# Kernel tuning notes

Measured on AMD Instinct MI355X. Metric: run time of the kernel, lower is better.

Reference implementation:

```python
import jax, jax.numpy as jnp
import numpy as np

EPS = 1e-5

def _layernorm(x, w, b):
    mu = jnp.mean(x, axis=-1, keepdims=True)
    var = jnp.var(x, axis=-1, keepdims=True)
    return (x - mu) * jax.lax.rsqrt(var + EPS) * w + b

def setup_inputs() -> dict:
    key = jax.random.key(0)
    ks = jax.random.split(key, 8)
    N, C = 768, 128
    s = 1.0 / np.sqrt(C)
    return {
        "pair": jax.random.normal(ks[0], (N, N, C), dtype=jnp.float32),
        "ln_in_w": jnp.ones((C,), jnp.float32),
        "ln_in_b": jnp.zeros((C,), jnp.float32),
        "w_proj": jax.random.uniform(ks[1], (2 * C, C), jnp.float32, -s, s),
        "w_gate": jax.random.uniform(ks[2], (2 * C, C), jnp.float32, -s, s),
        "ln_c_w": jnp.ones((C,), jnp.float32),
        "ln_c_b": jnp.zeros((C,), jnp.float32),
        "w_out": jax.random.uniform(ks[3], (C, C), jnp.float32, -s, s),
        "w_glin": jax.random.uniform(ks[4], (C, C), jnp.float32, -s, s),
    }

def reference(pair, ln_in_w, ln_in_b, w_proj, w_gate, ln_c_w, ln_c_b, w_out, w_glin):
    # pair: [N, N, C]
    x = _layernorm(pair, ln_in_w, ln_in_b)          # input LayerNorm
    proj = x @ w_proj.T                              # [N, N, 2C]
    gate = x @ w_gate.T                              # [N, N, 2C]
    pg = proj * jax.nn.sigmoid(gate)                 # gated projection
    # torch reshape([2C,N,N] -> [C,2,N,N]) interleaves channels:
    a = pg[..., 0::2]                                # [N, N, C]
    b = pg[..., 1::2]                                # [N, N, C]
    # outgoing: out[i,j,c] = sum_k a[i,k,c] * b[j,k,c]
    out = jnp.einsum('ikc,jkc->ijc', a, b)           # [N, N, C]
    out = _layernorm(out, ln_c_w, ln_c_b)
    out = out @ w_out.T
    out = out * jax.nn.sigmoid(x @ w_glin.T)         # output gate
    return out
```

## Files before the change

### kernel.cpp

```cpp
#include <hip/hip_runtime.h>
#include <stdint.h>


#define NN_F (768 * 768)

typedef float f32x4 __attribute__((ext_vector_type(4)));
typedef __bf16 bf16x8 __attribute__((ext_vector_type(8)));
typedef unsigned short u16x8 __attribute__((ext_vector_type(8)));

#define AS1 __attribute__((address_space(1)))
#define AS3 __attribute__((address_space(3)))

__device__ __forceinline__ unsigned short f2b(float f) {
  unsigned u = __builtin_bit_cast(unsigned, f);
  u = u + 0x7fffu + ((u >> 16) & 1u);
  return (unsigned short)(u >> 16);
}
__device__ __forceinline__ float b2f(unsigned short s) {
  return __builtin_bit_cast(float, ((unsigned)s) << 16);
}
__device__ __forceinline__ float sigf(float x) {
  return 1.0f / (1.0f + __expf(-x));
}

__global__ __launch_bounds__(256) void k0_weights(
    const float* __restrict__ w_proj, const float* __restrict__ w_gate,
    const float* __restrict__ w_glin, const float* __restrict__ w_out,
    unsigned short* __restrict__ Wcat) {
  int idx = blockIdx.x * 256 + threadIdx.x;
  int r = idx >> 7, k = idx & 127;
  float v;
  if (r < 512) {
    int c = r >> 2, tt = r & 3;
    int row = 2 * c + (tt >> 1);
    v = (tt & 1) ? w_gate[row * 128 + k] : w_proj[row * 128 + k];
  } else if (r < 640) {
    v = w_glin[(r - 512) * 128 + k];
  } else {
    v = w_out[(r - 640) * 128 + k];
  }
  Wcat[idx] = f2b(v);
}

__global__ __launch_bounds__(256) void k1_proj(
    const float* __restrict__ pair, const float* __restrict__ lnw,
    const float* __restrict__ lnb, const unsigned short* __restrict__ Wcat,
    unsigned short* __restrict__ a_t, unsigned short* __restrict__ b_t,
    unsigned short* __restrict__ g) {
  __shared__ float xs[64 * 132];
  __shared__ float red[8][64];
  __shared__ float muA[64], rsA[64];
  __shared__ unsigned short wbuf[32 * 512];

  const int t = threadIdx.x;
  const int l = t & 63, w = t >> 6;
  const int lm = l & 15, lq = l >> 4;
  const size_t p0 = (size_t)blockIdx.x * 64;

  const float* src = pair + p0 * 128;
#pragma unroll
  for (int v = 0; v < 8; ++v) {
    int fi = (v * 256 + t) * 4;
    int p = fi >> 7, c = fi & 127;
    f32x4 d = *(const f32x4*)(src + fi);
    *(f32x4*)&xs[p * 132 + c] = d;
  }
#pragma unroll
  for (int s0 = 0; s0 < 2; ++s0) {
    const int at = w * 2 + s0;
#pragma unroll
    for (int kt = 0; kt < 4; ++kt) {
      const unsigned short* gp =
          Wcat + (size_t)(at * 16 + lm) * 128 + kt * 32 + lq * 8;
      __builtin_amdgcn_global_load_lds((const AS1 void*)gp,
                                       (AS3 void*)(wbuf + (at * 4 + kt) * 512),
                                       16, 0, 0);
    }
  }
  __syncthreads();
  {
    int p = t & 63, q = t >> 6;
    float s1 = 0.f, s2 = 0.f;
#pragma unroll
    for (int cc = 0; cc < 32; ++cc) {
      float x = xs[p * 132 + q * 32 + ((cc + p) & 31)];
      s1 += x;
      s2 += x * x;
    }
    red[q][p] = s1;
    red[q + 4][p] = s2;
  }
  __syncthreads();
  if (t < 64) {
    float s1 = red[0][t] + red[1][t] + red[2][t] + red[3][t];
    float s2 = red[4][t] + red[5][t] + red[6][t] + red[7][t];
    float mu = s1 * (1.f / 128.f);
    float var = s2 * (1.f / 128.f) - mu * mu;
    muA[t] = mu;
    rsA[t] = rsqrtf(var + 1e-5f);
  }
  __syncthreads();
  bf16x8 xfr[4][4];
#pragma unroll
  for (int kt = 0; kt < 4; ++kt) {
    const int ks = kt * 32 + lq * 8;
    f32x4 w0 = *(const f32x4*)&lnw[ks];
    f32x4 w1 = *(const f32x4*)&lnw[ks + 4];
    f32x4 c0 = *(const f32x4*)&lnb[ks];
    f32x4 c1 = *(const f32x4*)&lnb[ks + 4];
#pragma unroll
    for (int pt = 0; pt < 4; ++pt) {
      const int p = pt * 16 + lm;
      float rs = rsA[p], nmu = -muA[p] * rs;
      f32x4 x0 = *(const f32x4*)&xs[p * 132 + ks];
      f32x4 x1 = *(const f32x4*)&xs[p * 132 + ks + 4];
      union { bf16x8 v; __bf16 e[8]; } fr;
#pragma unroll
      for (int j = 0; j < 4; ++j) {
        fr.e[j] = (__bf16)((x0[j] * rs + nmu) * w0[j] + c0[j]);
        fr.e[4 + j] = (__bf16)((x1[j] * rs + nmu) * w1[j] + c1[j]);
      }
      xfr[pt][kt] = fr.v;
    }
  }
  __builtin_amdgcn_sched_barrier(0);
#pragma unroll
  for (int s = 0; s < 10; ++s) {
    if (s >= 2 && s <= 8)
      __builtin_amdgcn_s_waitcnt(0x4f74);
    else if (s == 9)
      __builtin_amdgcn_s_waitcnt(0x0f7c);
    const int at = w * 2 + (s & 1);
    bf16x8 af[4];
#pragma unroll
    for (int kt = 0; kt < 4; ++kt)
      af[kt] = *(const bf16x8*)&wbuf[(at * 4 + kt) * 512 + l * 8];
    __builtin_amdgcn_s_waitcnt(0xc07f);
    __builtin_amdgcn_sched_barrier(0);
    if (s < 8) {
      const int r0n = ((s + 2) >> 1) * 128;
#pragma unroll
      for (int kt = 0; kt < 4; ++kt) {
        const unsigned short* gp =
            Wcat + (size_t)(r0n + at * 16 + lm) * 128 + kt * 32 + lq * 8;
        __builtin_amdgcn_global_load_lds(
            (const AS1 void*)gp, (AS3 void*)(wbuf + (at * 4 + kt) * 512),
            16, 0, 0);
      }
    }
    f32x4 acc[4];
#pragma unroll
    for (int pt = 0; pt < 4; ++pt) acc[pt] = (f32x4){0.f, 0.f, 0.f, 0.f};
#pragma unroll
    for (int pt = 0; pt < 4; ++pt)
#pragma unroll
      for (int kt = 0; kt < 4; ++kt)
        acc[pt] = __builtin_amdgcn_mfma_f32_16x16x32_bf16(af[kt], xfr[pt][kt],
                                                          acc[pt], 0, 0, 0);
    const int wc = s >> 1;
    const int rbase = wc * 128 + at * 16 + lq * 4;
#pragma unroll
    for (int pt = 0; pt < 4; ++pt) {
      f32x4 d = acc[pt];
      size_t point = p0 + pt * 16 + lm;
      if (wc < 4) {
        int c = rbase >> 2;
        a_t[(size_t)c * NN_F + point] = f2b(d[0] * sigf(d[1]));
        b_t[(size_t)c * NN_F + point] = f2b(d[2] * sigf(d[3]));
      } else {
        int co = rbase - 512;
        union { unsigned long long ll; unsigned short u[4]; } pk;
        pk.u[0] = f2b(sigf(d[0]));
        pk.u[1] = f2b(sigf(d[1]));
        pk.u[2] = f2b(sigf(d[2]));
        pk.u[3] = f2b(sigf(d[3]));
        *(unsigned long long*)&g[point * 128 + co] = pk.ll;
      }
    }
  }
}

__global__ __launch_bounds__(256) void k2_einsum(
    const unsigned short* __restrict__ a_t, const unsigned short* __restrict__ b_t,
    unsigned short* __restrict__ o_t) {
  __shared__ unsigned short As[2][128 * 32];
  __shared__ unsigned short Bs[2][128 * 32];
  const int t = threadIdx.x;
  const int l = t & 63, w = t >> 6;
  const int lm = l & 15, lq = l >> 4;
  const int c = blockIdx.z;
  const int m0 = blockIdx.y * 128, n0 = blockIdx.x * 128;
  const unsigned short* Ac = a_t + (size_t)c * NN_F;
  const unsigned short* Bc = b_t + (size_t)c * NN_F;
  const int wi = w >> 1, wj = w & 1;
  const int lrow = l >> 2, lk = (l & 3) * 8;
  f32x4 acc[4][4];
#pragma unroll
  for (int ti = 0; ti < 4; ++ti)
#pragma unroll
    for (int tj = 0; tj < 4; ++tj) acc[ti][tj] = (f32x4){0.f, 0.f, 0.f, 0.f};

  auto stage = [&](int buf, int kb) {
#pragma unroll
    for (int h = 0; h < 2; ++h) {
      int row = w * 32 + h * 16 + lrow;
      __builtin_amdgcn_global_load_lds(
          (const AS1 void*)(Ac + (size_t)(m0 + row) * 768 + kb * 32 + lk),
          (AS3 void*)(As[buf] + (w * 32 + h * 16) * 32), 16, 0, 0);
      __builtin_amdgcn_global_load_lds(
          (const AS1 void*)(Bc + (size_t)(n0 + row) * 768 + kb * 32 + lk),
          (AS3 void*)(Bs[buf] + (w * 32 + h * 16) * 32), 16, 0, 0);
    }
  };

  stage(0, 0);
  int cur = 0;
  for (int kb = 0; kb < 24; ++kb) {
    __syncthreads();
    if (kb < 23) stage(cur ^ 1, kb + 1);
    bf16x8 af[4], bfr[4];
#pragma unroll
    for (int ti = 0; ti < 4; ++ti)
      af[ti] = *(const bf16x8*)&As[cur][(wi * 64 + ti * 16 + lm) * 32 + lq * 8];
#pragma unroll
    for (int tj = 0; tj < 4; ++tj)
      bfr[tj] = *(const bf16x8*)&Bs[cur][(wj * 64 + tj * 16 + lm) * 32 + lq * 8];
#pragma unroll
    for (int ti = 0; ti < 4; ++ti)
#pragma unroll
      for (int tj = 0; tj < 4; ++tj)
        acc[ti][tj] = __builtin_amdgcn_mfma_f32_16x16x32_bf16(
            af[ti], bfr[tj], acc[ti][tj], 0, 0, 0);
    cur ^= 1;
  }
  unsigned short* Oc = o_t + (size_t)c * NN_F;
#pragma unroll
  for (int ti = 0; ti < 4; ++ti) {
    int ib = m0 + wi * 64 + ti * 16 + lq * 4;
#pragma unroll
    for (int tj = 0; tj < 4; ++tj) {
      int j = n0 + wj * 64 + tj * 16 + lm;
      f32x4 d = acc[ti][tj];
#pragma unroll
      for (int r = 0; r < 4; ++r) Oc[(size_t)(ib + r) * 768 + j] = f2b(d[r]);
    }
  }
}

__global__ __launch_bounds__(256) void k3_out(
    const unsigned short* __restrict__ o_t, const float* __restrict__ lnw,
    const float* __restrict__ lnb, const unsigned short* __restrict__ Wcat,
    const unsigned short* __restrict__ g, float* __restrict__ out) {
  __shared__ unsigned short ys[64 * 136];
  __shared__ float red[8][64];
  __shared__ float muA[64], rsA[64];
  __shared__ unsigned short wbuf[32 * 512];

  const int t = threadIdx.x;
  const int l = t & 63, w = t >> 6;
  const int lm = l & 15, lq = l >> 4;
  const size_t pblk = (size_t)blockIdx.x * 64;
  const int i = (int)(pblk / 768), j0 = (int)(pblk % 768);

#pragma unroll
  for (int at2 = 0; at2 < 2; ++at2) {
    int at = w * 2 + at2;
#pragma unroll
    for (int kt = 0; kt < 4; ++kt) {
      const unsigned short* gp =
          Wcat + (size_t)(640 + at * 16 + lm) * 128 + kt * 32 + lq * 8;
      __builtin_amdgcn_global_load_lds(
          (const AS1 void*)gp, (AS3 void*)(wbuf + (at * 4 + kt) * 512), 16, 0, 0);
    }
  }

  {
    const int jg = t & 7, cpb = t >> 3;
#pragma unroll
    for (int cg = 0; cg < 2; ++cg) {
      int cp = cg * 32 + cpb;
      const unsigned short* srcp =
          o_t + (size_t)(cp * 2) * NN_F + (size_t)i * 768 + j0 + jg * 8;
      u16x8 v0 = *(const u16x8*)srcp;
      u16x8 v1 = *(const u16x8*)(srcp + NN_F);
      int sp = cp ^ (jg << 2);
#pragma unroll
      for (int m = 0; m < 8; ++m) {
        unsigned pk = (unsigned)v0[m] | ((unsigned)v1[m] << 16);
        *(unsigned*)&ys[(jg * 8 + m) * 136 + sp * 2] = pk;
      }
    }
  }
  __syncthreads();
  {
    int p = t & 63, q = t >> 6;
    const unsigned* rowp = (const unsigned*)&ys[p * 136];
    float s1 = 0.f, s2 = 0.f;
#pragma unroll
    for (int ii = 0; ii < 16; ++ii) {
      unsigned pk = rowp[q * 16 + ((ii + p) & 15)];
      float xa = b2f((unsigned short)(pk & 0xffffu));
      float xb = b2f((unsigned short)(pk >> 16));
      s1 += xa + xb;
      s2 += xa * xa + xb * xb;
    }
    red[q][p] = s1;
    red[q + 4][p] = s2;
  }
  __syncthreads();
  if (t < 64) {
    float s1 = red[0][t] + red[1][t] + red[2][t] + red[3][t];
    float s2 = red[4][t] + red[5][t] + red[6][t] + red[7][t];
    float mu = s1 * (1.f / 128.f);
    float var = s2 * (1.f / 128.f) - mu * mu;
    muA[t] = mu;
    rsA[t] = rsqrtf(var + 1e-5f);
  }
  __syncthreads();
  bf16x8 yfr[4][4];
#pragma unroll
  for (int kt = 0; kt < 4; ++kt) {
    const int ks = kt * 32 + lq * 8;
    f32x4 w0 = *(const f32x4*)&lnw[ks];
    f32x4 w1 = *(const f32x4*)&lnw[ks + 4];
    f32x4 c0 = *(const f32x4*)&lnb[ks];
    f32x4 c1 = *(const f32x4*)&lnb[ks + 4];
    const int kp = ks >> 1;
#pragma unroll
    for (int pt = 0; pt < 4; ++pt) {
      const int p = pt * 16 + lm;
      float rs = rsA[p], nmu = -muA[p] * rs;
      int spos = (kp ^ ((p >> 3) << 2)) * 2;
      u16x8 raw = *(const u16x8*)&ys[p * 136 + spos];
      union { bf16x8 v; __bf16 e[8]; } fr;
#pragma unroll
      for (int j = 0; j < 4; ++j) {
        float x0 = b2f(raw[j]);
        float x1 = b2f(raw[4 + j]);
        fr.e[j] = (__bf16)((x0 * rs + nmu) * w0[j] + c0[j]);
        fr.e[4 + j] = (__bf16)((x1 * rs + nmu) * w1[j] + c1[j]);
      }
      yfr[pt][kt] = fr.v;
    }
  }
  __builtin_amdgcn_s_waitcnt(0x0f70);
  f32x4 acc[2][4];
#pragma unroll
  for (int a2 = 0; a2 < 2; ++a2)
#pragma unroll
    for (int pt = 0; pt < 4; ++pt) acc[a2][pt] = (f32x4){0.f, 0.f, 0.f, 0.f};
#pragma unroll
  for (int at2 = 0; at2 < 2; ++at2) {
    int at = w * 2 + at2;
    bf16x8 af[4];
#pragma unroll
    for (int kt = 0; kt < 4; ++kt)
      af[kt] = *(const bf16x8*)&wbuf[(at * 4 + kt) * 512 + l * 8];
#pragma unroll
    for (int pt = 0; pt < 4; ++pt)
#pragma unroll
      for (int kt = 0; kt < 4; ++kt)
        acc[at2][pt] = __builtin_amdgcn_mfma_f32_16x16x32_bf16(
            af[kt], yfr[pt][kt], acc[at2][pt], 0, 0, 0);
  }
#pragma unroll
  for (int at2 = 0; at2 < 2; ++at2) {
    int ob = (w * 2 + at2) * 16 + lq * 4;
#pragma unroll
    for (int pt = 0; pt < 4; ++pt) {
      size_t point = pblk + pt * 16 + lm;
      f32x4 d = acc[at2][pt];
      union { unsigned long long ll; unsigned short u[4]; } pk;
      pk.ll = *(const unsigned long long*)(g + point * 128 + ob);
      f32x4 r;
      r[0] = d[0] * b2f(pk.u[0]);
      r[1] = d[1] * b2f(pk.u[1]);
      r[2] = d[2] * b2f(pk.u[2]);
      r[3] = d[3] * b2f(pk.u[3]);
      *(f32x4*)&out[point * 128 + ob] = r;
    }
  }
}

extern "C" void kernel_launch(void* const* d_in, const int* in_sizes, int n_in,
                              void* d_out, int out_size, void* d_ws, size_t ws_size,
                              hipStream_t stream) {
  const float* pair = (const float*)d_in[0];
  const float* ln_in_w = (const float*)d_in[1];
  const float* ln_in_b = (const float*)d_in[2];
  const float* w_proj = (const float*)d_in[3];
  const float* w_gate = (const float*)d_in[4];
  const float* ln_c_w = (const float*)d_in[5];
  const float* ln_c_b = (const float*)d_in[6];
  const float* w_out = (const float*)d_in[7];
  const float* w_glin = (const float*)d_in[8];
  float* out = (float*)d_out;

  char* ws = (char*)d_ws;
  const size_t SZ = (size_t)150994944;
  unsigned short* a_t = (unsigned short*)(ws);
  unsigned short* b_t = (unsigned short*)(ws + SZ);
  unsigned short* o_t = (unsigned short*)(ws + 2 * SZ);
  unsigned short* g = (unsigned short*)(ws + 3 * SZ);
  unsigned short* Wcat = (unsigned short*)(ws + 4 * SZ);

  hipLaunchKernelGGL(k0_weights, dim3(384), dim3(256), 0, stream,
                     w_proj, w_gate, w_glin, w_out, Wcat);
  hipLaunchKernelGGL(k1_proj, dim3(9216), dim3(256), 0, stream,
                     pair, ln_in_w, ln_in_b, Wcat, a_t, b_t, g);
  hipLaunchKernelGGL(k2_einsum, dim3(6, 6, 128), dim3(256), 0, stream,
                     a_t, b_t, o_t);
  hipLaunchKernelGGL(k3_out, dim3(9216), dim3(256), 0, stream,
                     o_t, ln_c_w, ln_c_b, Wcat, g, out);
}
```

Measured before the change: 1.145 ms.

## Drop LDS staging in proj and out kernels, raise occupancy bounds

In k1_proj the 33KB LDS tile of the input rows is removed. LayerNorm statistics are now computed straight from global loads, using a 4-lane shuffle reduction, and the normalization reads the input again from global memory. In k3_out the weight staging through LDS is removed and A fragments are loaded directly from global. Both kernels gain a min-blocks-per-CU hint of 4. The aim is lower LDS use and fewer barriers so more blocks fit per CU, at the cost of reading the pair tensor twice from global/L2 and possible register pressure.

Result: slower. 1.386 ms (+21.0%).

```diff
diff --git a/kernel.cpp b/kernel.cpp
--- a/kernel.cpp
+++ b/kernel.cpp
@@ -42,13 +42,11 @@
   Wcat[idx] = f2b(v);
 }
 
-__global__ __launch_bounds__(256) void k1_proj(
+__global__ __launch_bounds__(256, 4) void k1_proj(
     const float* __restrict__ pair, const float* __restrict__ lnw,
     const float* __restrict__ lnb, const unsigned short* __restrict__ Wcat,
     unsigned short* __restrict__ a_t, unsigned short* __restrict__ b_t,
     unsigned short* __restrict__ g) {
-  __shared__ float xs[64 * 132];
-  __shared__ float red[8][64];
   __shared__ float muA[64], rsA[64];
   __shared__ unsigned short wbuf[32 * 512];
 
@@ -56,15 +54,8 @@
   const int l = t & 63, w = t >> 6;
   const int lm = l & 15, lq = l >> 4;
   const size_t p0 = (size_t)blockIdx.x * 64;
-
   const float* src = pair + p0 * 128;
-#pragma unroll
-  for (int v = 0; v < 8; ++v) {
-    int fi = (v * 256 + t) * 4;
-    int p = fi >> 7, c = fi & 127;
-    f32x4 d = *(const f32x4*)(src + fi);
-    *(f32x4*)&xs[p * 132 + c] = d;
-  }
+
 #pragma unroll
   for (int s0 = 0; s0 < 2; ++s0) {
     const int at = w * 2 + s0;
@@ -77,29 +68,33 @@
                                        16, 0, 0);
     }
   }
+
+  {
+    const int r = w * 16 + (l >> 2), q = l & 3;
+    const float* rp = src + r * 128;
+    float s1 = 0.f, s2 = 0.f;
+#pragma unroll
+    for (int e = 0; e < 8; ++e) {
+      f32x4 v = *(const f32x4*)(rp + (q + e * 4) * 4);
+#pragma unroll
+      for (int j = 0; j < 4; ++j) {
+        s1 += v[j];
+        s2 += v[j] * v[j];
+      }
+    }
+    s1 += __shfl_xor(s1, 1);
+    s2 += __shfl_xor(s2, 1);
+    s1 += __shfl_xor(s1, 2);
+    s2 += __shfl_xor(s2, 2);
+    if (q == 0) {
+      float mu = s1 * (1.f / 128.f);
+      float var = s2 * (1.f / 128.f) - mu * mu;
+      muA[r] = mu;
+      rsA[r] = rsqrtf(var + 1e-5f);
+    }
+  }
   __syncthreads();
-  {
-    int p = t & 63, q = t >> 6;
-    float s1 = 0.f, s2 = 0.f;
-#pragma unroll
-    for (int cc = 0; cc < 32; ++cc) {
-      float x = xs[p * 132 + q * 32 + ((cc + p) & 31)];
-      s1 += x;
-      s2 += x * x;
-    }
-    red[q][p] = s1;
-    red[q + 4][p] = s2;
-  }
-  __syncthreads();
-  if (t < 64) {
-    float s1 = red[0][t] + red[1][t] + red[2][t] + red[3][t];
-    float s2 = red[4][t] + red[5][t] + red[6][t] + red[7][t];
-    float mu = s1 * (1.f / 128.f);
-    float var = s2 * (1.f / 128.f) - mu * mu;
-    muA[t] = mu;
-    rsA[t] = rsqrtf(var + 1e-5f);
-  }
-  __syncthreads();
+
   bf16x8 xfr[4][4];
 #pragma unroll
   for (int kt = 0; kt < 4; ++kt) {
@@ -112,8 +107,9 @@
     for (int pt = 0; pt < 4; ++pt) {
       const int p = pt * 16 + lm;
       float rs = rsA[p], nmu = -muA[p] * rs;
-      f32x4 x0 = *(const f32x4*)&xs[p * 132 + ks];
-      f32x4 x1 = *(const f32x4*)&xs[p * 132 + ks + 4];
+      const float* xp = src + p * 128 + ks;
+      f32x4 x0 = *(const f32x4*)xp;
+      f32x4 x1 = *(const f32x4*)(xp + 4);
       union { bf16x8 v; __bf16 e[8]; } fr;
 #pragma unroll
       for (int j = 0; j < 4; ++j) {
@@ -247,32 +243,19 @@
   }
 }
 
-__global__ __launch_bounds__(256) void k3_out(
+__global__ __launch_bounds__(256, 4) void k3_out(
     const unsigned short* __restrict__ o_t, const float* __restrict__ lnw,
     const float* __restrict__ lnb, const unsigned short* __restrict__ Wcat,
     const unsigned short* __restrict__ g, float* __restrict__ out) {
   __shared__ unsigned short ys[64 * 136];
   __shared__ float red[8][64];
   __shared__ float muA[64], rsA[64];
-  __shared__ unsigned short wbuf[32 * 512];
 
   const int t = threadIdx.x;
   const int l = t & 63, w = t >> 6;
   const int lm = l & 15, lq = l >> 4;
   const size_t pblk = (size_t)blockIdx.x * 64;
   const int i = (int)(pblk / 768), j0 = (int)(pblk % 768);
-
-#pragma unroll
-  for (int at2 = 0; at2 < 2; ++at2) {
-    int at = w * 2 + at2;
-#pragma unroll
-    for (int kt = 0; kt < 4; ++kt) {
-      const unsigned short* gp =
-          Wcat + (size_t)(640 + at * 16 + lm) * 128 + kt * 32 + lq * 8;
-      __builtin_amdgcn_global_load_lds(
-          (const AS1 void*)gp, (AS3 void*)(wbuf + (at * 4 + kt) * 512), 16, 0, 0);
-    }
-  }
 
   {
     const int jg = t & 7, cpb = t >> 3;
@@ -343,33 +326,28 @@
       yfr[pt][kt] = fr.v;
     }
   }
-  __builtin_amdgcn_s_waitcnt(0x0f70);
-  f32x4 acc[2][4];
-#pragma unroll
-  for (int a2 = 0; a2 < 2; ++a2)
-#pragma unroll
-    for (int pt = 0; pt < 4; ++pt) acc[a2][pt] = (f32x4){0.f, 0.f, 0.f, 0.f};
 #pragma unroll
   for (int at2 = 0; at2 < 2; ++at2) {
-    int at = w * 2 + at2;
+    const int at = w * 2 + at2;
     bf16x8 af[4];
 #pragma unroll
     for (int kt = 0; kt < 4; ++kt)
-      af[kt] = *(const bf16x8*)&wbuf[(at * 4 + kt) * 512 + l * 8];
+      af[kt] = *(const bf16x8*)(Wcat + (size_t)(640 + at * 16 + lm) * 128 +
+                                kt * 32 + lq * 8);
+    f32x4 acc[4];
+#pragma unroll
+    for (int pt = 0; pt < 4; ++pt) acc[pt] = (f32x4){0.f, 0.f, 0.f, 0.f};
 #pragma unroll
     for (int pt = 0; pt < 4; ++pt)
 #pragma unroll
       for (int kt = 0; kt < 4; ++kt)
-        acc[at2][pt] = __builtin_amdgcn_mfma_f32_16x16x32_bf16(
-            af[kt], yfr[pt][kt], acc[at2][pt], 0, 0, 0);
-  }
-#pragma unroll
-  for (int at2 = 0; at2 < 2; ++at2) {
-    int ob = (w * 2 + at2) * 16 + lq * 4;
+        acc[pt] = __builtin_amdgcn_mfma_f32_16x16x32_bf16(af[kt], yfr[pt][kt],
+                                                          acc[pt], 0, 0, 0);
+    const int ob = at * 16 + lq * 4;
 #pragma unroll
     for (int pt = 0; pt < 4; ++pt) {
       size_t point = pblk + pt * 16 + lm;
-      f32x4 d = acc[at2][pt];
+      f32x4 d = acc[pt];
       union { unsigned long long ll; unsigned short u[4]; } pk;
       pk.ll = *(const unsigned long long*)(g + point * 128 + ob);
       f32x4 r;
```

## Drop LDS weight staging, read weights from global, remap einsum blocks for XCD locality

Applied to the files above, without the earlier changes.

k1_proj and k3_out no longer stage weight tiles in shared memory through async global-to-LDS copies. Weight fragments are now read straight from global memory (expected to hit L2), with launch_bounds raised to request 4 blocks per CU, so the kernels use less LDS and can keep more blocks resident. k2_einsum switches to a 1D grid whose block IDs are remapped so that consecutive blocks on the same XCD (bid & 7) work on the same channel, aiming for better L2 reuse of a_t and b_t. In exchange the explicit prefetch pipelining of weights is lost, and the weight loads may add latency.

New measurement: 1.077 ms. 1.06x faster.

```diff
diff --git a/kernel.cpp b/kernel.cpp
--- a/kernel.cpp
+++ b/kernel.cpp
@@ -42,7 +42,7 @@
   Wcat[idx] = f2b(v);
 }
 
-__global__ __launch_bounds__(256) void k1_proj(
+__global__ __launch_bounds__(256, 4) void k1_proj(
     const float* __restrict__ pair, const float* __restrict__ lnw,
     const float* __restrict__ lnb, const unsigned short* __restrict__ Wcat,
     unsigned short* __restrict__ a_t, unsigned short* __restrict__ b_t,
@@ -50,7 +50,6 @@
   __shared__ float xs[64 * 132];
   __shared__ float red[8][64];
   __shared__ float muA[64], rsA[64];
-  __shared__ unsigned short wbuf[32 * 512];
 
   const int t = threadIdx.x;
   const int l = t & 63, w = t >> 6;
@@ -64,18 +63,6 @@
     int p = fi >> 7, c = fi & 127;
     f32x4 d = *(const f32x4*)(src + fi);
     *(f32x4*)&xs[p * 132 + c] = d;
-  }
-#pragma unroll
-  for (int s0 = 0; s0 < 2; ++s0) {
-    const int at = w * 2 + s0;
-#pragma unroll
-    for (int kt = 0; kt < 4; ++kt) {
-      const unsigned short* gp =
-          Wcat + (size_t)(at * 16 + lm) * 128 + kt * 32 + lq * 8;
-      __builtin_amdgcn_global_load_lds((const AS1 void*)gp,
-                                       (AS3 void*)(wbuf + (at * 4 + kt) * 512),
-                                       16, 0, 0);
-    }
   }
   __syncthreads();
   {
@@ -123,31 +110,16 @@
       xfr[pt][kt] = fr.v;
     }
   }
-  __builtin_amdgcn_sched_barrier(0);
 #pragma unroll
   for (int s = 0; s < 10; ++s) {
-    if (s >= 2 && s <= 8)
-      __builtin_amdgcn_s_waitcnt(0x4f74);
-    else if (s == 9)
-      __builtin_amdgcn_s_waitcnt(0x0f7c);
     const int at = w * 2 + (s & 1);
+    const int wc = s >> 1;
+    const int r0 = wc * 128;
     bf16x8 af[4];
 #pragma unroll
     for (int kt = 0; kt < 4; ++kt)
-      af[kt] = *(const bf16x8*)&wbuf[(at * 4 + kt) * 512 + l * 8];
-    __builtin_amdgcn_s_waitcnt(0xc07f);
-    __builtin_amdgcn_sched_barrier(0);
-    if (s < 8) {
-      const int r0n = ((s + 2) >> 1) * 128;
-#pragma unroll
-      for (int kt = 0; kt < 4; ++kt) {
-        const unsigned short* gp =
-            Wcat + (size_t)(r0n + at * 16 + lm) * 128 + kt * 32 + lq * 8;
-        __builtin_amdgcn_global_load_lds(
-            (const AS1 void*)gp, (AS3 void*)(wbuf + (at * 4 + kt) * 512),
-            16, 0, 0);
-      }
-    }
+      af[kt] = *(const bf16x8*)(Wcat + (size_t)(r0 + at * 16 + lm) * 128 +
+                                kt * 32 + lq * 8);
     f32x4 acc[4];
 #pragma unroll
     for (int pt = 0; pt < 4; ++pt) acc[pt] = (f32x4){0.f, 0.f, 0.f, 0.f};
@@ -157,8 +129,7 @@
       for (int kt = 0; kt < 4; ++kt)
         acc[pt] = __builtin_amdgcn_mfma_f32_16x16x32_bf16(af[kt], xfr[pt][kt],
                                                           acc[pt], 0, 0, 0);
-    const int wc = s >> 1;
-    const int rbase = wc * 128 + at * 16 + lq * 4;
+    const int rbase = r0 + at * 16 + lq * 4;
 #pragma unroll
     for (int pt = 0; pt < 4; ++pt) {
       f32x4 d = acc[pt];
@@ -188,8 +159,11 @@
   const int t = threadIdx.x;
   const int l = t & 63, w = t >> 6;
   const int lm = l & 15, lq = l >> 4;
-  const int c = blockIdx.z;
-  const int m0 = blockIdx.y * 128, n0 = blockIdx.x * 128;
+  const int bid = blockIdx.x;
+  const int nb = (bid & 7) * 576 + (bid >> 3);
+  const int c = nb / 36;
+  const int rem = nb % 36;
+  const int m0 = (rem / 6) * 128, n0 = (rem % 6) * 128;
   const unsigned short* Ac = a_t + (size_t)c * NN_F;
   const unsigned short* Bc = b_t + (size_t)c * NN_F;
   const int wi = w >> 1, wj = w & 1;
@@ -247,32 +221,19 @@
   }
 }
 
-__global__ __launch_bounds__(256) void k3_out(
+__global__ __launch_bounds__(256, 4) void k3_out(
     const unsigned short* __restrict__ o_t, const float* __restrict__ lnw,
     const float* __restrict__ lnb, const unsigned short* __restrict__ Wcat,
     const unsigned short* __restrict__ g, float* __restrict__ out) {
   __shared__ unsigned short ys[64 * 136];
   __shared__ float red[8][64];
   __shared__ float muA[64], rsA[64];
-  __shared__ unsigned short wbuf[32 * 512];
 
   const int t = threadIdx.x;
   const int l = t & 63, w = t >> 6;
   const int lm = l & 15, lq = l >> 4;
   const size_t pblk = (size_t)blockIdx.x * 64;
   const int i = (int)(pblk / 768), j0 = (int)(pblk % 768);
-
-#pragma unroll
-  for (int at2 = 0; at2 < 2; ++at2) {
-    int at = w * 2 + at2;
-#pragma unroll
-    for (int kt = 0; kt < 4; ++kt) {
-      const unsigned short* gp =
-          Wcat + (size_t)(640 + at * 16 + lm) * 128 + kt * 32 + lq * 8;
-      __builtin_amdgcn_global_load_lds(
-          (const AS1 void*)gp, (AS3 void*)(wbuf + (at * 4 + kt) * 512), 16, 0, 0);
-    }
-  }
 
   {
     const int jg = t & 7, cpb = t >> 3;
@@ -343,33 +304,28 @@
       yfr[pt][kt] = fr.v;
     }
   }
-  __builtin_amdgcn_s_waitcnt(0x0f70);
-  f32x4 acc[2][4];
-#pragma unroll
-  for (int a2 = 0; a2 < 2; ++a2)
-#pragma unroll
-    for (int pt = 0; pt < 4; ++pt) acc[a2][pt] = (f32x4){0.f, 0.f, 0.f, 0.f};
 #pragma unroll
   for (int at2 = 0; at2 < 2; ++at2) {
-    int at = w * 2 + at2;
+    const int at = w * 2 + at2;
     bf16x8 af[4];
 #pragma unroll
     for (int kt = 0; kt < 4; ++kt)
-      af[kt] = *(const bf16x8*)&wbuf[(at * 4 + kt) * 512 + l * 8];
+      af[kt] = *(const bf16x8*)(Wcat + (size_t)(640 + at * 16 + lm) * 128 +
+                                kt * 32 + lq * 8);
+    f32x4 acc[4];
+#pragma unroll
+    for (int pt = 0; pt < 4; ++pt) acc[pt] = (f32x4){0.f, 0.f, 0.f, 0.f};
 #pragma unroll
     for (int pt = 0; pt < 4; ++pt)
 #pragma unroll
       for (int kt = 0; kt < 4; ++kt)
-        acc[at2][pt] = __builtin_amdgcn_mfma_f32_16x16x32_bf16(
-            af[kt], yfr[pt][kt], acc[at2][pt], 0, 0, 0);
-  }
-#pragma unroll
-  for (int at2 = 0; at2 < 2; ++at2) {
-    int ob = (w * 2 + at2) * 16 + lq * 4;
+        acc[pt] = __builtin_amdgcn_mfma_f32_16x16x32_bf16(af[kt], yfr[pt][kt],
+                                                          acc[pt], 0, 0, 0);
+    const int ob = at * 16 + lq * 4;
 #pragma unroll
     for (int pt = 0; pt < 4; ++pt) {
       size_t point = pblk + pt * 16 + lm;
-      f32x4 d = acc[at2][pt];
+      f32x4 d = acc[pt];
       union { unsigned long long ll; unsigned short u[4]; } pk;
       pk.ll = *(const unsigned long long*)(g + point * 128 + ob);
       f32x4 r;
@@ -408,7 +364,7 @@
                      w_proj, w_gate, w_glin, w_out, Wcat);
   hipLaunchKernelGGL(k1_proj, dim3(9216), dim3(256), 0, stream,
                      pair, ln_in_w, ln_in_b, Wcat, a_t, b_t, g);
-  hipLaunchKernelGGL(k2_einsum, dim3(6, 6, 128), dim3(256), 0, stream,
+  hipLaunchKernelGGL(k2_einsum, dim3(4608), dim3(256), 0, stream,
                      a_t, b_t, o_t);
   hipLaunchKernelGGL(k3_out, dim3(9216), dim3(256), 0, stream,
                      o_t, ln_c_w, ln_c_b, Wcat, g, out);
```
